# Kernel tuning notes

Measured on AMD Instinct MI355X. Metric: run time of the kernel, lower is better.

The kernel has to match this reference:

```python
import jax, jax.numpy as jnp
import numpy as np

N, E, F_IN, H, C = 50000, 800000, 128, 4, 73
HC = H * C  # 292
NEG_SLOPE_ATT = 0.2   # GATv2 attention leaky relu
NEG_SLOPE_ACT = 0.01  # F.leaky_relu default
BN_EPS = 1e-5


def setup_inputs() -> dict:
    key = jax.random.key(0)
    ks = jax.random.split(key, 20)
    rn = lambda k, shp, s=0.05: (jax.random.normal(k, shp, jnp.float32) * s)
    inp = {
        'x': jax.random.normal(ks[0], (N, F_IN), jnp.float32),
        'edge_index': jax.random.randint(ks[1], (2, E), 0, N, jnp.int64),
        # conv1 (in=F_IN)
        'Wl1': rn(ks[2], (HC, F_IN)), 'bl1': rn(ks[3], (HC,)),
        'Wr1': rn(ks[4], (HC, F_IN)), 'br1': rn(ks[5], (HC,)),
        'att1': rn(ks[6], (H, C)), 'b1': rn(ks[7], (HC,)),
        # conv2 (in=HC)
        'Wl2': rn(ks[8], (HC, HC)), 'bl2': rn(ks[9], (HC,)),
        'Wr2': rn(ks[10], (HC, HC)), 'br2': rn(ks[11], (HC,)),
        'att2': rn(ks[12], (H, C)), 'b2': rn(ks[13], (HC,)),
        # shared BatchNorm1d(HC)
        'gamma': jnp.ones((HC,), jnp.float32), 'beta': jnp.zeros((HC,), jnp.float32),
        # classifier Linear(HC, 2)
        'Wc': rn(ks[14], (2, HC)), 'bc': rn(ks[15], (2,)),
    }
    return inp


def _gatv2(x, src, dst, Wl, bl, Wr, br, att, b):
    # lin_l on source, lin_r on target (PyG GATv2Conv, share_weights=False)
    xl = (x @ Wl.T + bl).reshape(-1, H, C)  # [N,H,C]
    xr = (x @ Wr.T + br).reshape(-1, H, C)
    f = xl[src] + xr[dst]                    # [E,H,C] edge-wise gather
    s = jnp.einsum('ehc,hc->eh', jax.nn.leaky_relu(f, NEG_SLOPE_ATT), att)
    # segment softmax over incoming edges of each destination node
    m = jax.ops.segment_max(s, dst, num_segments=N)
    ex = jnp.exp(s - m[dst])
    den = jax.ops.segment_sum(ex, dst, num_segments=N)
    alpha = ex / (den[dst] + 1e-16)          # [E,H]
    out = jax.ops.segment_sum(alpha[:, :, None] * xl[src], dst, num_segments=N)
    return out.reshape(-1, HC) + b           # concat heads + bias


def _bn(x, gamma, beta):
    mu = jnp.mean(x, axis=0)
    var = jnp.mean((x - mu) ** 2, axis=0)
    return (x - mu) * jax.lax.rsqrt(var + BN_EPS) * gamma + beta


def reference(x, edge_index, Wl1, bl1, Wr1, br1, att1, b1,
              Wl2, bl2, Wr2, br2, att2, b2, gamma, beta, Wc, bc):
    src, dst = edge_index[0], edge_index[1]
    h = _gatv2(x, src, dst, Wl1, bl1, Wr1, br1, att1, b1)
    h = jax.nn.leaky_relu(_bn(h, gamma, beta), NEG_SLOPE_ACT)
    h = _gatv2(h, src, dst, Wl2, bl2, Wr2, br2, att2, b2)
    h = jax.nn.leaky_relu(_bn(h, gamma, beta), NEG_SLOPE_ACT)
    return h @ Wc.T + bc
```

## Files before the change

kernel.cpp:

```cpp
#include <hip/hip_runtime.h>

#define HCDIM 292
#define NHEAD 4
#define CDIM 73
#define SLOTS 5
#define NPERM 320
#define BN_EPS 1e-5f

using u16x8 = __attribute__((ext_vector_type(8))) unsigned short;
using s16x8 = __attribute__((ext_vector_type(8))) short;
using f32x4 = __attribute__((ext_vector_type(4))) float;
using u16x4 = __attribute__((ext_vector_type(4))) unsigned short;

__device__ inline ushort f2bf(float f) {
  unsigned int u = __float_as_uint(f);
  u += 0x7FFFu + ((u >> 16) & 1u);
  return (ushort)(u >> 16);
}
__device__ inline float bf2f(ushort v) {
  return __uint_as_float(((unsigned int)v) << 16);
}

__device__ inline int perm2feat(int p, bool& valid) {
  int h, c;
  if (p < 256) {
    h = p >> 6;
    c = ((p & 3) << 4) | ((p >> 2) & 15);
    valid = true;
  } else {
    int q = p - 256;
    h = q >> 4;
    c = 64 + (q & 15);
    valid = (q & 15) < (CDIM - 64);
  }
  return h * CDIM + c;
}

__global__ void k_wperm(const float* __restrict__ W, const float* __restrict__ b,
                        ushort* __restrict__ Wp, float* __restrict__ pb,
                        int Kin, int Kpad, int kperm) {
  int p = blockIdx.x, t = threadIdx.x;
  bool pv;
  int gn = perm2feat(p, pv);
  int gk = t;
  bool kv = t < Kin;
  if (kperm) { bool v2; gk = perm2feat(t, v2); kv = v2; }
  ushort v = 0;
  if (pv && kv) v = f2bf(W[(size_t)gn * Kin + gk]);
  Wp[(size_t)p * Kpad + t] = v;
  if (t == 0) pb[p] = pv ? b[gn] : 0.f;
}

__global__ void k_vecperm(const float* __restrict__ att1, const float* __restrict__ b1,
                          const float* __restrict__ att2, const float* __restrict__ b2,
                          const float* __restrict__ gamma, const float* __restrict__ beta,
                          const float* __restrict__ Wc, float* __restrict__ o) {
  int p = threadIdx.x, w = blockIdx.x;
  bool pv;
  int gn = perm2feat(p, pv);
  const float* src;
  switch (w) {
    case 0: src = att1; break;
    case 1: src = b1; break;
    case 2: src = att2; break;
    case 3: src = b2; break;
    case 4: src = gamma; break;
    case 5: src = beta; break;
    case 6: src = Wc; break;
    default: src = Wc + HCDIM; break;
  }
  o[w * NPERM + p] = pv ? src[gn] : 0.f;
}

__global__ void k_hist(const int* __restrict__ dst, int* __restrict__ deg, int E) {
  int i = blockIdx.x * blockDim.x + threadIdx.x;
  if (i < E) atomicAdd(&deg[dst[i]], 1);
}

__global__ __launch_bounds__(256) void k_block_sum(const int* __restrict__ deg,
                                                   int* __restrict__ bsum, int n) {
  __shared__ int s[256];
  int i = blockIdx.x * 256 + threadIdx.x;
  s[threadIdx.x] = (i < n) ? deg[i] : 0;
  __syncthreads();
  for (int off = 128; off > 0; off >>= 1) {
    if (threadIdx.x < off) s[threadIdx.x] += s[threadIdx.x + off];
    __syncthreads();
  }
  if (threadIdx.x == 0) bsum[blockIdx.x] = s[0];
}

__global__ __launch_bounds__(256) void k_scan_small(const int* __restrict__ bsum,
                                                    int* __restrict__ boff, int G) {
  __shared__ int s[256];
  int t = threadIdx.x;
  int v = (t < G) ? bsum[t] : 0;
  s[t] = v;
  __syncthreads();
  for (int off = 1; off < 256; off <<= 1) {
    int tv = (t >= off) ? s[t - off] : 0;
    __syncthreads();
    s[t] += tv;
    __syncthreads();
  }
  if (t < G) boff[t] = s[t] - v;
}

__global__ __launch_bounds__(256) void k_scan_final(const int* __restrict__ deg,
                                                    const int* __restrict__ boff,
                                                    int* __restrict__ row_ptr,
                                                    int* __restrict__ cursor,
                                                    int n, int E) {
  __shared__ int s[256];
  int t = threadIdx.x;
  int i = blockIdx.x * 256 + t;
  int v = (i < n) ? deg[i] : 0;
  s[t] = v;
  __syncthreads();
  for (int off = 1; off < 256; off <<= 1) {
    int tv = (t >= off) ? s[t - off] : 0;
    __syncthreads();
    s[t] += tv;
    __syncthreads();
  }
  if (i < n) {
    int rp = boff[blockIdx.x] + s[t] - v;
    row_ptr[i] = rp;
    cursor[i] = rp;
  }
  if (i == 0) row_ptr[n] = E;
}

__global__ void k_csr_fill(const int* __restrict__ srcs, const int* __restrict__ dsts,
                           int* __restrict__ cursor, int* __restrict__ csr_src, int E) {
  int i = blockIdx.x * blockDim.x + threadIdx.x;
  if (i < E) {
    int pos = atomicAdd(&cursor[dsts[i]], 1);
    csr_src[pos] = srcs[i];
  }
}

template <bool CVT>
__device__ inline void load_af(const char* const (&Ar)[4], int koff, int quad,
                               s16x8 (&af)[4]) {
#pragma unroll
  for (int i = 0; i < 4; ++i) {
    if (CVT) {
      const float* p = (const float*)Ar[i] + koff + quad * 8;
      float4 f0 = *(const float4*)p;
      float4 f1 = *(const float4*)(p + 4);
      s16x8 v;
      v[0] = (short)f2bf(f0.x); v[1] = (short)f2bf(f0.y);
      v[2] = (short)f2bf(f0.z); v[3] = (short)f2bf(f0.w);
      v[4] = (short)f2bf(f1.x); v[5] = (short)f2bf(f1.y);
      v[6] = (short)f2bf(f1.z); v[7] = (short)f2bf(f1.w);
      af[i] = v;
    } else {
      af[i] = *(const s16x8*)((const ushort*)Ar[i] + koff + quad * 8);
    }
  }
}

template <int KS, bool CVT>
__global__ __launch_bounds__(256) void k_gemm_blds(
    const void* __restrict__ Av, const ushort* __restrict__ Wb,
    const float* __restrict__ pb, ushort* __restrict__ o0,
    ushort* __restrict__ o1, int M, int miters) {
  constexpr int KSTEPS = KS / 32;
  constexpr int BSTR = KS + 8;
  __shared__ ushort Bs[80 * BSTR];
  int b = blockIdx.x;
  int mlo = b & 7, ct = (b >> 3) & 7, mhi = b >> 6;
  int mc = mlo + 8 * mhi;
  ushort* out = (ct < 4) ? o0 : o1;
  const int colbase = (ct & 3) * 80;
  const int tid = threadIdx.x;
  const int wave = tid >> 6, lane = tid & 63;
  const int quad = lane >> 4, lr = lane & 15;
  const int esz = CVT ? 4 : 2;

  for (int idx = tid; idx < 80 * (KS / 8); idx += 256) {
    int r = idx / (KS / 8), c8 = idx - r * (KS / 8);
    *(u16x8*)(Bs + r * BSTR + c8 * 8) =
        *(const u16x8*)(Wb + (size_t)(ct * 80 + r) * KS + c8 * 8);
  }
  __syncthreads();

  const ushort* bp[5];
#pragma unroll
  for (int i = 0; i < 5; ++i) bp[i] = Bs + (i * 16 + lr) * BSTR;

  float4 pbv[5];
#pragma unroll
  for (int ni = 0; ni < 5; ++ni)
    pbv[ni] = *(const float4*)(pb + ct * 80 + ni * 16 + quad * 4);

  for (int it = mc; it < miters; it += 64) {
    int mbase = it * 256 + wave * 64;
    const char* Ar[4];
#pragma unroll
    for (int i = 0; i < 4; ++i) {
      int ar = mbase + i * 16 + lr;
      if (ar >= M) ar = M - 1;
      Ar[i] = (const char*)Av + (size_t)ar * KS * esz;
    }
    f32x4 acc[4][5] = {};
    s16x8 afb[2][4];
    load_af<CVT>(Ar, 0, quad, afb[0]);
#pragma unroll
    for (int s = 0; s < KSTEPS; ++s) {
      if (s + 1 < KSTEPS) load_af<CVT>(Ar, (s + 1) * 32, quad, afb[(s + 1) & 1]);
      s16x8 bf[5];
#pragma unroll
      for (int i = 0; i < 5; ++i)
        bf[i] = *(const s16x8*)(bp[i] + s * 32 + quad * 8);
#pragma unroll
      for (int ni = 0; ni < 5; ++ni)
#pragma unroll
        for (int mi = 0; mi < 4; ++mi)
          acc[mi][ni] = __builtin_amdgcn_mfma_f32_16x16x32_bf16(
              bf[ni], afb[s & 1][mi], acc[mi][ni], 0, 0, 0);
    }
#pragma unroll
    for (int mi = 0; mi < 4; ++mi) {
      int gm = mbase + mi * 16 + lr;
      if (gm >= M) continue;
      ushort* orow = out + (size_t)gm * NPERM + colbase + quad * 4;
#pragma unroll
      for (int ni = 0; ni < 5; ++ni) {
        u16x4 o;
        o[0] = f2bf(acc[mi][ni][0] + pbv[ni].x);
        o[1] = f2bf(acc[mi][ni][1] + pbv[ni].y);
        o[2] = f2bf(acc[mi][ni][2] + pbv[ni].z);
        o[3] = f2bf(acc[mi][ni][3] + pbv[ni].w);
        *(u16x4*)(orow + ni * 16) = o;
      }
    }
  }
}

__global__ __launch_bounds__(256) void k_pre(const ushort* __restrict__ xl,
                                             const float* __restrict__ attp,
                                             float* __restrict__ pl, int n) {
  int wave = threadIdx.x >> 6, lane = threadIdx.x & 63;
  int d = blockIdx.x * 4 + wave;
  if (d >= n) return;
  int hgrp = lane >> 4, li = lane & 15;
  u16x4 a4 = *(const u16x4*)(xl + (size_t)d * NPERM + lane * 4);
  ushort a1 = xl[(size_t)d * NPERM + 256 + lane];
  float Ta = 0.f;
#pragma unroll
  for (int k = 0; k < 4; ++k) Ta = fmaf(bf2f(a4[k]), attp[lane * 4 + k], Ta);
  Ta = fmaf(bf2f(a1), attp[256 + lane], Ta);
#pragma unroll
  for (int off = 1; off < 16; off <<= 1) Ta += __shfl_xor(Ta, off, 64);
  if (li == 0) pl[d * 4 + hgrp] = 0.6f * Ta;
}

__global__ __launch_bounds__(256) void k_agg(const ushort* __restrict__ xl,
                                             const ushort* __restrict__ xr,
                                             const float* __restrict__ pl,
                                             const int* __restrict__ csr_src,
                                             const int* __restrict__ row_ptr,
                                             const float* __restrict__ attp,
                                             const float* __restrict__ bp,
                                             ushort* __restrict__ out, int n) {
  int wave = threadIdx.x >> 6, lane = threadIdx.x & 63;
  int d = blockIdx.x * 4 + wave;
  if (d >= n) return;
  int hgrp = lane >> 4;
  int start = __builtin_amdgcn_readfirstlane(row_ptr[d]);
  int end = __builtin_amdgcn_readfirstlane(row_ptr[d + 1]);

  float bpv[SLOTS];
#pragma unroll
  for (int k = 0; k < 4; ++k) bpv[k] = bp[lane * 4 + k];
  bpv[4] = bp[256 + lane];

  if (start >= end) {
    u16x4 o4;
#pragma unroll
    for (int k = 0; k < 4; ++k) o4[k] = f2bf(bpv[k]);
    *(u16x4*)(out + (size_t)d * NPERM + lane * 4) = o4;
    out[(size_t)d * NPERM + 256 + lane] = f2bf(bpv[4]);
    return;
  }

  float xrv[SLOTS], attv[SLOTS], acc[SLOTS] = {};
  {
    u16x4 r4 = *(const u16x4*)(xr + (size_t)d * NPERM + lane * 4);
#pragma unroll
    for (int k = 0; k < 4; ++k) {
      xrv[k] = bf2f(r4[k]);
      attv[k] = 0.4f * attp[lane * 4 + k];
    }
    xrv[4] = bf2f(xr[(size_t)d * NPERM + 256 + lane]);
    attv[4] = 0.4f * attp[256 + lane];
  }
  float Tb = 0.f;
#pragma unroll
  for (int k = 0; k < SLOTS; ++k) Tb = fmaf(xrv[k], attv[k], Tb);
  Tb += __shfl_xor(Tb, 1, 64);
  Tb += __shfl_xor(Tb, 2, 64);
  Tb += __shfl_xor(Tb, 4, 64);
  Tb += __shfl_xor(Tb, 8, 64);
  float prv = 1.5f * Tb;
  float den = 0.f;
  int dg = end - start;

  int sA = __builtin_amdgcn_readfirstlane(csr_src[start]);
  int eB0 = (dg > 1) ? start + 1 : start;
  int sB = __builtin_amdgcn_readfirstlane(csr_src[eB0]);
  u16x4 a4 = *(const u16x4*)(xl + (size_t)sA * NPERM + lane * 4);
  ushort a1 = xl[(size_t)sA * NPERM + 256 + lane];
  float plA = pl[sA * 4 + hgrp];
  u16x4 b4 = *(const u16x4*)(xl + (size_t)sB * NPERM + lane * 4);
  ushort b1 = xl[(size_t)sB * NPERM + 256 + lane];
  float plB = pl[sB * 4 + hgrp];

  for (int e = start; e + 1 < end; e += 2) {
    int p0 = (e + 2 < end) ? e + 2 : end - 1;
    int p1 = (e + 3 < end) ? e + 3 : end - 1;
    int t0 = __builtin_amdgcn_readfirstlane(csr_src[p0]);
    int t1 = __builtin_amdgcn_readfirstlane(csr_src[p1]);
    u16x4 n4a = *(const u16x4*)(xl + (size_t)t0 * NPERM + lane * 4);
    ushort n1a = xl[(size_t)t0 * NPERM + 256 + lane];
    float plN0 = pl[t0 * 4 + hgrp];
    u16x4 n4b = *(const u16x4*)(xl + (size_t)t1 * NPERM + lane * 4);
    ushort n1b = xl[(size_t)t1 * NPERM + 256 + lane];
    float plN1 = pl[t1 * 4 + hgrp];

    float xa[SLOTS] = {bf2f(a4[0]), bf2f(a4[1]), bf2f(a4[2]), bf2f(a4[3]), bf2f(a1)};
    float xb[SLOTS] = {bf2f(b4[0]), bf2f(b4[1]), bf2f(b4[2]), bf2f(b4[3]), bf2f(b1)};
    float Ta = 0.f, Tc = 0.f;
#pragma unroll
    for (int k = 0; k < SLOTS; ++k) {
      Ta = fmaf(fabsf(xa[k] + xrv[k]), attv[k], Ta);
      Tc = fmaf(fabsf(xb[k] + xrv[k]), attv[k], Tc);
    }
    Ta += __shfl_xor(Ta, 1, 64);  Tc += __shfl_xor(Tc, 1, 64);
    Ta += __shfl_xor(Ta, 2, 64);  Tc += __shfl_xor(Tc, 2, 64);
    Ta += __shfl_xor(Ta, 4, 64);  Tc += __shfl_xor(Tc, 4, 64);
    Ta += __shfl_xor(Ta, 8, 64);  Tc += __shfl_xor(Tc, 8, 64);
    float sa_ = fminf(Ta + plA + prv, 60.f);
    float sb_ = fminf(Tc + plB + prv, 60.f);
    float wa = __expf(sa_);
    float wb = __expf(sb_);
    den += wa + wb;
#pragma unroll
    for (int k = 0; k < SLOTS; ++k) {
      acc[k] = fmaf(wa, xa[k], acc[k]);
      acc[k] = fmaf(wb, xb[k], acc[k]);
    }
    a4 = n4a; a1 = n1a; plA = plN0;
    b4 = n4b; b1 = n1b; plB = plN1;
  }

  if (dg & 1) {
    float xa[SLOTS] = {bf2f(a4[0]), bf2f(a4[1]), bf2f(a4[2]), bf2f(a4[3]), bf2f(a1)};
    float Ta = 0.f;
#pragma unroll
    for (int k = 0; k < SLOTS; ++k)
      Ta = fmaf(fabsf(xa[k] + xrv[k]), attv[k], Ta);
    Ta += __shfl_xor(Ta, 1, 64);
    Ta += __shfl_xor(Ta, 2, 64);
    Ta += __shfl_xor(Ta, 4, 64);
    Ta += __shfl_xor(Ta, 8, 64);
    float wa = __expf(fminf(Ta + plA + prv, 60.f));
    den += wa;
#pragma unroll
    for (int k = 0; k < SLOTS; ++k) acc[k] = fmaf(wa, xa[k], acc[k]);
  }

  float inv = 1.f / (den + 1e-16f);
  u16x4 o4;
#pragma unroll
  for (int k = 0; k < 4; ++k) o4[k] = f2bf(fmaf(acc[k], inv, bpv[k]));
  *(u16x4*)(out + (size_t)d * NPERM + lane * 4) = o4;
  out[(size_t)d * NPERM + 256 + lane] = f2bf(fmaf(acc[4], inv, bpv[4]));
}

__global__ __launch_bounds__(320) void k_bn_reduce(const ushort* __restrict__ h,
                                                   float* __restrict__ colsum,
                                                   float* __restrict__ colsq,
                                                   int n, int rows_per_block) {
  int c = threadIdx.x;
  int r0 = blockIdx.x * rows_per_block;
  int r1 = min(r0 + rows_per_block, n);
  float s = 0.f, s2 = 0.f;
  for (int r = r0; r < r1; ++r) {
    float v = bf2f(h[(size_t)r * NPERM + c]);
    s += v;
    s2 += v * v;
  }
  atomicAdd(&colsum[c], s);
  atomicAdd(&colsq[c], s2);
}

__global__ void k_bn_coef(float* __restrict__ colsum, float* __restrict__ colsq,
                          const float* __restrict__ gp, const float* __restrict__ bp,
                          float invN) {
  int c = threadIdx.x + blockIdx.x * blockDim.x;
  if (c >= NPERM) return;
  float mu = colsum[c] * invN;
  float var = colsq[c] * invN - mu * mu;
  float scale = rsqrtf(var + BN_EPS) * gp[c];
  colsum[c] = scale;
  colsq[c] = bp[c] - mu * scale;
}

__global__ void k_bn_apply_bf(const ushort* __restrict__ h,
                              const float* __restrict__ scale,
                              const float* __restrict__ shift,
                              ushort* __restrict__ outb, int total8) {
  int i = blockIdx.x * blockDim.x + threadIdx.x;
  if (i >= total8) return;
  int cg = i - (i / 40) * 40;
  u16x8 v = *(const u16x8*)(h + (size_t)i * 8);
  u16x8 o;
#pragma unroll
  for (int k = 0; k < 8; ++k) {
    int c = cg * 8 + k;
    float f = fmaf(bf2f(v[k]), scale[c], shift[c]);
    f = (f > 0.f) ? f : 0.01f * f;
    o[k] = f2bf(f);
  }
  *(u16x8*)(outb + (size_t)i * 8) = o;
}

__global__ __launch_bounds__(256) void k_bn_classifier(
    const ushort* __restrict__ h, const float* __restrict__ scale,
    const float* __restrict__ shift, const float* __restrict__ wc0,
    const float* __restrict__ wc1, const float* __restrict__ bc,
    float* __restrict__ out, int n) {
  int wave = threadIdx.x >> 6, lane = threadIdx.x & 63;
  int r = blockIdx.x * 4 + wave;
  if (r >= n) return;
  float a0 = 0.f, a1 = 0.f;
#pragma unroll
  for (int k = 0; k < SLOTS; ++k) {
    int slot = lane + 64 * k;
    float v = fmaf(bf2f(h[(size_t)r * NPERM + slot]), scale[slot], shift[slot]);
    v = (v > 0.f) ? v : 0.01f * v;
    a0 = fmaf(v, wc0[slot], a0);
    a1 = fmaf(v, wc1[slot], a1);
  }
#pragma unroll
  for (int off = 32; off > 0; off >>= 1) {
    a0 += __shfl_xor(a0, off, 64);
    a1 += __shfl_xor(a1, off, 64);
  }
  if (lane == 0) {
    out[(size_t)2 * r] = a0 + bc[0];
    out[(size_t)2 * r + 1] = a1 + bc[1];
  }
}

extern "C" void kernel_launch(void* const* d_in, const int* in_sizes, int n_in,
                              void* d_out, int out_size, void* d_ws, size_t ws_size,
                              hipStream_t stream) {
  const float* x      = (const float*)d_in[0];
  const int*   eidx   = (const int*)d_in[1];
  const float* Wl1    = (const float*)d_in[2];
  const float* bl1    = (const float*)d_in[3];
  const float* Wr1    = (const float*)d_in[4];
  const float* br1    = (const float*)d_in[5];
  const float* att1   = (const float*)d_in[6];
  const float* b1     = (const float*)d_in[7];
  const float* Wl2    = (const float*)d_in[8];
  const float* bl2    = (const float*)d_in[9];
  const float* Wr2    = (const float*)d_in[10];
  const float* br2    = (const float*)d_in[11];
  const float* att2   = (const float*)d_in[12];
  const float* b2     = (const float*)d_in[13];
  const float* gamma  = (const float*)d_in[14];
  const float* beta   = (const float*)d_in[15];
  const float* Wc     = (const float*)d_in[16];
  const float* bc     = (const float*)d_in[17];
  float* out = (float*)d_out;

  const int FIN = 128;
  const int N = in_sizes[0] / FIN;
  const int E = in_sizes[1] / 2;

  const int* src = eidx;
  const int* dst = eidx + E;

  ushort* h      = (ushort*)d_ws;
  ushort* xl     = h + (size_t)N * NPERM;
  ushort* xr     = xl + (size_t)N * NPERM;
  ushort* abuf   = xr + (size_t)N * NPERM;
  ushort* wb     = abuf + (size_t)N * NPERM;
  float* pb      = (float*)(wb + (size_t)2 * NPERM * NPERM);
  float* vecp    = pb + 2 * NPERM;
  float* pl      = vecp + 8 * NPERM;
  float* colsum  = pl + (size_t)N * NHEAD;
  float* colsq   = colsum + NPERM;
  int* deg       = (int*)(colsq + NPERM);
  int* row_ptr   = deg + N;
  int* cursor    = row_ptr + N + 1;
  int* bsum      = cursor + N;
  int* boff      = bsum + 256;
  int* csr_src   = boff + 256;

  const int G = (N + 255) / 256;
  const int EB = (E + 255) / 256;
  const int AGGB = (N + 3) / 4;
  const int MITERS = (N + 255) / 256;
  const int GEMMB = 512;

  const float* att1p = vecp;
  const float* b1p   = vecp + NPERM;
  const float* att2p = vecp + 2 * NPERM;
  const float* b2p   = vecp + 3 * NPERM;
  const float* gp    = vecp + 4 * NPERM;
  const float* btp   = vecp + 5 * NPERM;
  const float* wc0   = vecp + 6 * NPERM;
  const float* wc1   = vecp + 7 * NPERM;

  hipMemsetAsync(deg, 0, (size_t)N * sizeof(int), stream);
  k_hist<<<EB, 256, 0, stream>>>(dst, deg, E);
  k_block_sum<<<G, 256, 0, stream>>>(deg, bsum, N);
  k_scan_small<<<1, 256, 0, stream>>>(bsum, boff, G);
  k_scan_final<<<G, 256, 0, stream>>>(deg, boff, row_ptr, cursor, N, E);
  k_csr_fill<<<EB, 256, 0, stream>>>(src, dst, cursor, csr_src, E);

  k_vecperm<<<8, NPERM, 0, stream>>>(att1, b1, att2, b2, gamma, beta, Wc, vecp);

  k_wperm<<<NPERM, FIN, 0, stream>>>(Wl1, bl1, wb, pb, FIN, FIN, 0);
  k_wperm<<<NPERM, FIN, 0, stream>>>(Wr1, br1, wb + (size_t)NPERM * FIN, pb + NPERM,
                                     FIN, FIN, 0);
  k_gemm_blds<FIN, true><<<GEMMB, 256, 0, stream>>>((const void*)x, wb, pb,
                                                    xl, xr, N, MITERS);
  k_pre<<<AGGB, 256, 0, stream>>>(xl, att1p, pl, N);
  k_agg<<<AGGB, 256, 0, stream>>>(xl, xr, pl, csr_src, row_ptr, att1p, b1p, h, N);

  const int RPB = (N + 255) / 256;
  hipMemsetAsync(colsum, 0, 2 * NPERM * sizeof(float), stream);
  k_bn_reduce<<<256, NPERM, 0, stream>>>(h, colsum, colsq, N, RPB);
  k_bn_coef<<<2, 160, 0, stream>>>(colsum, colsq, gp, btp, 1.f / (float)N);
  k_bn_apply_bf<<<(N * 40 + 255) / 256, 256, 0, stream>>>(h, colsum, colsq, abuf,
                                                          N * 40);

  k_wperm<<<NPERM, NPERM, 0, stream>>>(Wl2, bl2, wb, pb, HCDIM, NPERM, 1);
  k_wperm<<<NPERM, NPERM, 0, stream>>>(Wr2, br2, wb + (size_t)NPERM * NPERM,
                                       pb + NPERM, HCDIM, NPERM, 1);
  k_gemm_blds<NPERM, false><<<GEMMB, 256, 0, stream>>>((const void*)abuf, wb, pb,
                                                       xl, xr, N, MITERS);
  k_pre<<<AGGB, 256, 0, stream>>>(xl, att2p, pl, N);
  k_agg<<<AGGB, 256, 0, stream>>>(xl, xr, pl, csr_src, row_ptr, att2p, b2p, h, N);

  hipMemsetAsync(colsum, 0, 2 * NPERM * sizeof(float), stream);
  k_bn_reduce<<<256, NPERM, 0, stream>>>(h, colsum, colsq, N, RPB);
  k_bn_coef<<<2, 160, 0, stream>>>(colsum, colsq, gp, btp, 1.f / (float)N);

  k_bn_classifier<<<AGGB, 256, 0, stream>>>(h, colsum, colsq, wc0, wc1, bc, out, N);
}
```

Measured before the change: 635.2 us.

## Switch intermediate storage and MFMA from bf16 to fp16 with packed dot math

Changes every stored intermediate (weights, projected features, aggregated outputs) from bf16 to fp16. The GEMMs now use fp16 MFMA and packed round-toward-zero conversion instead of manual bf16 rounding. The attention logits in the aggregation kernel use packed half adds, abs via bitmask and fdot2, and the softmax uses exp2 with log2e folded into the attention vector. This cuts conversion and ALU instructions in the edge loop. The trade-off is fp16 range and precision risk on activations, and the exp clamp threshold changes.

```diff
diff --git a/kernel.cpp b/kernel.cpp
--- a/kernel.cpp
+++ b/kernel.cpp
@@ -6,19 +6,32 @@
 #define SLOTS 5
 #define NPERM 320
 #define BN_EPS 1e-5f
+#define LOG2E 1.44269504f
 
 using u16x8 = __attribute__((ext_vector_type(8))) unsigned short;
-using s16x8 = __attribute__((ext_vector_type(8))) short;
 using f32x4 = __attribute__((ext_vector_type(4))) float;
 using u16x4 = __attribute__((ext_vector_type(4))) unsigned short;
-
-__device__ inline ushort f2bf(float f) {
-  unsigned int u = __float_as_uint(f);
-  u += 0x7FFFu + ((u >> 16) & 1u);
-  return (ushort)(u >> 16);
-}
-__device__ inline float bf2f(ushort v) {
-  return __uint_as_float(((unsigned int)v) << 16);
+using hf2   = __attribute__((ext_vector_type(2))) _Float16;
+using v2h   = __attribute__((ext_vector_type(2))) __fp16;
+using v8h   = __attribute__((ext_vector_type(8))) __fp16;
+
+__device__ inline v2h pkrtz(float a, float b) {
+  return __builtin_amdgcn_cvt_pkrtz(a, b);
+}
+__device__ inline float fdot2(hf2 a, hf2 b, float c) {
+  return __builtin_amdgcn_fdot2(__builtin_bit_cast(v2h, a),
+                                __builtin_bit_cast(v2h, b), c, false);
+}
+__device__ inline ushort f2h(float f) {
+  _Float16 h = (_Float16)f;
+  return __builtin_bit_cast(ushort, h);
+}
+__device__ inline float h2f(ushort v) {
+  return (float)__builtin_bit_cast(_Float16, v);
+}
+__device__ inline hf2 habs2(hf2 a) {
+  unsigned u = __builtin_bit_cast(unsigned, a) & 0x7fff7fffu;
+  return __builtin_bit_cast(hf2, u);
 }
 
 __device__ inline int perm2feat(int p, bool& valid) {
@@ -46,7 +59,7 @@
   bool kv = t < Kin;
   if (kperm) { bool v2; gk = perm2feat(t, v2); kv = v2; }
   ushort v = 0;
-  if (pv && kv) v = f2bf(W[(size_t)gn * Kin + gk]);
+  if (pv && kv) v = f2h(W[(size_t)gn * Kin + gk]);
   Wp[(size_t)p * Kpad + t] = v;
   if (t == 0) pb[p] = pv ? b[gn] : 0.f;
 }
@@ -142,21 +155,21 @@
 
 template <bool CVT>
 __device__ inline void load_af(const char* const (&Ar)[4], int koff, int quad,
-                               s16x8 (&af)[4]) {
+                               v8h (&af)[4]) {
 #pragma unroll
   for (int i = 0; i < 4; ++i) {
     if (CVT) {
       const float* p = (const float*)Ar[i] + koff + quad * 8;
       float4 f0 = *(const float4*)p;
       float4 f1 = *(const float4*)(p + 4);
-      s16x8 v;
-      v[0] = (short)f2bf(f0.x); v[1] = (short)f2bf(f0.y);
-      v[2] = (short)f2bf(f0.z); v[3] = (short)f2bf(f0.w);
-      v[4] = (short)f2bf(f1.x); v[5] = (short)f2bf(f1.y);
-      v[6] = (short)f2bf(f1.z); v[7] = (short)f2bf(f1.w);
-      af[i] = v;
+      union { v2h h[4]; v8h v; } u;
+      u.h[0] = pkrtz(f0.x, f0.y);
+      u.h[1] = pkrtz(f0.z, f0.w);
+      u.h[2] = pkrtz(f1.x, f1.y);
+      u.h[3] = pkrtz(f1.z, f1.w);
+      af[i] = u.v;
     } else {
-      af[i] = *(const s16x8*)((const ushort*)Ar[i] + koff + quad * 8);
+      af[i] = *(const v8h*)((const ushort*)Ar[i] + koff + quad * 8);
     }
   }
 }
@@ -205,20 +218,20 @@
       Ar[i] = (const char*)Av + (size_t)ar * KS * esz;
     }
     f32x4 acc[4][5] = {};
-    s16x8 afb[2][4];
+    v8h afb[2][4];
     load_af<CVT>(Ar, 0, quad, afb[0]);
 #pragma unroll
     for (int s = 0; s < KSTEPS; ++s) {
       if (s + 1 < KSTEPS) load_af<CVT>(Ar, (s + 1) * 32, quad, afb[(s + 1) & 1]);
-      s16x8 bf[5];
+      v8h bf[5];
 #pragma unroll
       for (int i = 0; i < 5; ++i)
-        bf[i] = *(const s16x8*)(bp[i] + s * 32 + quad * 8);
+        bf[i] = *(const v8h*)(bp[i] + s * 32 + quad * 8);
 #pragma unroll
       for (int ni = 0; ni < 5; ++ni)
 #pragma unroll
         for (int mi = 0; mi < 4; ++mi)
-          acc[mi][ni] = __builtin_amdgcn_mfma_f32_16x16x32_bf16(
+          acc[mi][ni] = __builtin_amdgcn_mfma_f32_16x16x32_f16(
               bf[ni], afb[s & 1][mi], acc[mi][ni], 0, 0, 0);
     }
 #pragma unroll
@@ -228,12 +241,10 @@
       ushort* orow = out + (size_t)gm * NPERM + colbase + quad * 4;
 #pragma unroll
       for (int ni = 0; ni < 5; ++ni) {
-        u16x4 o;
-        o[0] = f2bf(acc[mi][ni][0] + pbv[ni].x);
-        o[1] = f2bf(acc[mi][ni][1] + pbv[ni].y);
-        o[2] = f2bf(acc[mi][ni][2] + pbv[ni].z);
-        o[3] = f2bf(acc[mi][ni][3] + pbv[ni].w);
-        *(u16x4*)(orow + ni * 16) = o;
+        union { v2h h[2]; u16x4 o; } u;
+        u.h[0] = pkrtz(acc[mi][ni][0] + pbv[ni].x, acc[mi][ni][1] + pbv[ni].y);
+        u.h[1] = pkrtz(acc[mi][ni][2] + pbv[ni].z, acc[mi][ni][3] + pbv[ni].w);
+        *(u16x4*)(orow + ni * 16) = u.o;
       }
     }
   }
@@ -246,15 +257,22 @@
   int d = blockIdx.x * 4 + wave;
   if (d >= n) return;
   int hgrp = lane >> 4, li = lane & 15;
-  u16x4 a4 = *(const u16x4*)(xl + (size_t)d * NPERM + lane * 4);
-  ushort a1 = xl[(size_t)d * NPERM + 256 + lane];
-  float Ta = 0.f;
-#pragma unroll
-  for (int k = 0; k < 4; ++k) Ta = fmaf(bf2f(a4[k]), attp[lane * 4 + k], Ta);
-  Ta = fmaf(bf2f(a1), attp[256 + lane], Ta);
+  const float C = 0.4f * LOG2E;
+  float4 a4 = *(const float4*)(attp + lane * 4);
+  hf2 av01{(_Float16)(C * a4.x), (_Float16)(C * a4.y)};
+  hf2 av23{(_Float16)(C * a4.z), (_Float16)(C * a4.w)};
+  hf2 av5{(_Float16)(C * attp[256 + lane]), (_Float16)0.f};
+
+  uint2 cc = *(const uint2*)(xl + (size_t)d * NPERM + lane * 4);
+  ushort c5 = xl[(size_t)d * NPERM + 256 + lane];
+  hf2 c01 = __builtin_bit_cast(hf2, cc.x);
+  hf2 c23 = __builtin_bit_cast(hf2, cc.y);
+  hf2 c5h{__builtin_bit_cast(_Float16, c5), (_Float16)0.f};
+
+  float Ta = fdot2(c01, av01, fdot2(c23, av23, fdot2(c5h, av5, 0.f)));
 #pragma unroll
   for (int off = 1; off < 16; off <<= 1) Ta += __shfl_xor(Ta, off, 64);
-  if (li == 0) pl[d * 4 + hgrp] = 0.6f * Ta;
+  if (li == 0) pl[d * 4 + hgrp] = 1.5f * Ta;
 }
 
 __global__ __launch_bounds__(256) void k_agg(const ushort* __restrict__ xl,
@@ -272,49 +290,49 @@
   int start = __builtin_amdgcn_readfirstlane(row_ptr[d]);
   int end = __builtin_amdgcn_readfirstlane(row_ptr[d + 1]);
 
-  float bpv[SLOTS];
-#pragma unroll
-  for (int k = 0; k < 4; ++k) bpv[k] = bp[lane * 4 + k];
-  bpv[4] = bp[256 + lane];
+  float4 bp4 = *(const float4*)(bp + lane * 4);
+  float bp5 = bp[256 + lane];
 
   if (start >= end) {
-    u16x4 o4;
-#pragma unroll
-    for (int k = 0; k < 4; ++k) o4[k] = f2bf(bpv[k]);
-    *(u16x4*)(out + (size_t)d * NPERM + lane * 4) = o4;
-    out[(size_t)d * NPERM + 256 + lane] = f2bf(bpv[4]);
+    union { v2h h[2]; u16x4 o; } u;
+    u.h[0] = pkrtz(bp4.x, bp4.y);
+    u.h[1] = pkrtz(bp4.z, bp4.w);
+    *(u16x4*)(out + (size_t)d * NPERM + lane * 4) = u.o;
+    out[(size_t)d * NPERM + 256 + lane] = f2h(bp5);
     return;
   }
 
-  float xrv[SLOTS], attv[SLOTS], acc[SLOTS] = {};
+  const float C = 0.4f * LOG2E;
+  float4 at4 = *(const float4*)(attp + lane * 4);
+  hf2 av01{(_Float16)(C * at4.x), (_Float16)(C * at4.y)};
+  hf2 av23{(_Float16)(C * at4.z), (_Float16)(C * at4.w)};
+  hf2 av5{(_Float16)(C * attp[256 + lane]), (_Float16)0.f};
+
+  hf2 xr01, xr23, xr5;
   {
-    u16x4 r4 = *(const u16x4*)(xr + (size_t)d * NPERM + lane * 4);
-#pragma unroll
-    for (int k = 0; k < 4; ++k) {
-      xrv[k] = bf2f(r4[k]);
-      attv[k] = 0.4f * attp[lane * 4 + k];
-    }
-    xrv[4] = bf2f(xr[(size_t)d * NPERM + 256 + lane]);
-    attv[4] = 0.4f * attp[256 + lane];
-  }
-  float Tb = 0.f;
-#pragma unroll
-  for (int k = 0; k < SLOTS; ++k) Tb = fmaf(xrv[k], attv[k], Tb);
+    uint2 rr = *(const uint2*)(xr + (size_t)d * NPERM + lane * 4);
+    xr01 = __builtin_bit_cast(hf2, rr.x);
+    xr23 = __builtin_bit_cast(hf2, rr.y);
+    xr5 = hf2{__builtin_bit_cast(_Float16, xr[(size_t)d * NPERM + 256 + lane]),
+              (_Float16)0.f};
+  }
+  float Tb = fdot2(xr01, av01, fdot2(xr23, av23, fdot2(xr5, av5, 0.f)));
   Tb += __shfl_xor(Tb, 1, 64);
   Tb += __shfl_xor(Tb, 2, 64);
   Tb += __shfl_xor(Tb, 4, 64);
   Tb += __shfl_xor(Tb, 8, 64);
   float prv = 1.5f * Tb;
+  float acc[SLOTS] = {};
   float den = 0.f;
   int dg = end - start;
 
   int sA = __builtin_amdgcn_readfirstlane(csr_src[start]);
   int eB0 = (dg > 1) ? start + 1 : start;
   int sB = __builtin_amdgcn_readfirstlane(csr_src[eB0]);
-  u16x4 a4 = *(const u16x4*)(xl + (size_t)sA * NPERM + lane * 4);
+  uint2 a8 = *(const uint2*)(xl + (size_t)sA * NPERM + lane * 4);
   ushort a1 = xl[(size_t)sA * NPERM + 256 + lane];
   float plA = pl[sA * 4 + hgrp];
-  u16x4 b4 = *(const u16x4*)(xl + (size_t)sB * NPERM + lane * 4);
+  uint2 b8 = *(const uint2*)(xl + (size_t)sB * NPERM + lane * 4);
   ushort b1 = xl[(size_t)sB * NPERM + 256 + lane];
   float plB = pl[sB * 4 + hgrp];
 
@@ -323,61 +341,70 @@
     int p1 = (e + 3 < end) ? e + 3 : end - 1;
     int t0 = __builtin_amdgcn_readfirstlane(csr_src[p0]);
     int t1 = __builtin_amdgcn_readfirstlane(csr_src[p1]);
-    u16x4 n4a = *(const u16x4*)(xl + (size_t)t0 * NPERM + lane * 4);
+    uint2 n8a = *(const uint2*)(xl + (size_t)t0 * NPERM + lane * 4);
     ushort n1a = xl[(size_t)t0 * NPERM + 256 + lane];
     float plN0 = pl[t0 * 4 + hgrp];
-    u16x4 n4b = *(const u16x4*)(xl + (size_t)t1 * NPERM + lane * 4);
+    uint2 n8b = *(const uint2*)(xl + (size_t)t1 * NPERM + lane * 4);
     ushort n1b = xl[(size_t)t1 * NPERM + 256 + lane];
     float plN1 = pl[t1 * 4 + hgrp];
 
-    float xa[SLOTS] = {bf2f(a4[0]), bf2f(a4[1]), bf2f(a4[2]), bf2f(a4[3]), bf2f(a1)};
-    float xb[SLOTS] = {bf2f(b4[0]), bf2f(b4[1]), bf2f(b4[2]), bf2f(b4[3]), bf2f(b1)};
-    float Ta = 0.f, Tc = 0.f;
-#pragma unroll
-    for (int k = 0; k < SLOTS; ++k) {
-      Ta = fmaf(fabsf(xa[k] + xrv[k]), attv[k], Ta);
-      Tc = fmaf(fabsf(xb[k] + xrv[k]), attv[k], Tc);
-    }
+    hf2 a01 = __builtin_bit_cast(hf2, a8.x), a23 = __builtin_bit_cast(hf2, a8.y);
+    hf2 a5{__builtin_bit_cast(_Float16, a1), (_Float16)0.f};
+    hf2 c01 = __builtin_bit_cast(hf2, b8.x), c23 = __builtin_bit_cast(hf2, b8.y);
+    hf2 c5{__builtin_bit_cast(_Float16, b1), (_Float16)0.f};
+
+    float Ta = fdot2(habs2(a01 + xr01), av01,
+               fdot2(habs2(a23 + xr23), av23,
+               fdot2(habs2(a5 + xr5), av5, 0.f)));
+    float Tc = fdot2(habs2(c01 + xr01), av01,
+               fdot2(habs2(c23 + xr23), av23,
+               fdot2(habs2(c5 + xr5), av5, 0.f)));
     Ta += __shfl_xor(Ta, 1, 64);  Tc += __shfl_xor(Tc, 1, 64);
     Ta += __shfl_xor(Ta, 2, 64);  Tc += __shfl_xor(Tc, 2, 64);
     Ta += __shfl_xor(Ta, 4, 64);  Tc += __shfl_xor(Tc, 4, 64);
     Ta += __shfl_xor(Ta, 8, 64);  Tc += __shfl_xor(Tc, 8, 64);
-    float sa_ = fminf(Ta + plA + prv, 60.f);
-    float sb_ = fminf(Tc + plB + prv, 60.f);
-    float wa = __expf(sa_);
-    float wb = __expf(sb_);
+    float wa = exp2f(fminf(Ta + plA + prv, 80.f));
+    float wb = exp2f(fminf(Tc + plB + prv, 80.f));
     den += wa + wb;
-#pragma unroll
-    for (int k = 0; k < SLOTS; ++k) {
-      acc[k] = fmaf(wa, xa[k], acc[k]);
-      acc[k] = fmaf(wb, xb[k], acc[k]);
-    }
-    a4 = n4a; a1 = n1a; plA = plN0;
-    b4 = n4b; b1 = n1b; plB = plN1;
+    acc[0] = fmaf(wa, (float)a01[0], acc[0]);
+    acc[1] = fmaf(wa, (float)a01[1], acc[1]);
+    acc[2] = fmaf(wa, (float)a23[0], acc[2]);
+    acc[3] = fmaf(wa, (float)a23[1], acc[3]);
+    acc[4] = fmaf(wa, (float)a5[0], acc[4]);
+    acc[0] = fmaf(wb, (float)c01[0], acc[0]);
+    acc[1] = fmaf(wb, (float)c01[1], acc[1]);
+    acc[2] = fmaf(wb, (float)c23[0], acc[2]);
+    acc[3] = fmaf(wb, (float)c23[1], acc[3]);
+    acc[4] = fmaf(wb, (float)c5[0], acc[4]);
+    a8 = n8a; a1 = n1a; plA = plN0;
+    b8 = n8b; b1 = n1b; plB = plN1;
   }
 
   if (dg & 1) {
-    float xa[SLOTS] = {bf2f(a4[0]), bf2f(a4[1]), bf2f(a4[2]), bf2f(a4[3]), bf2f(a1)};
-    float Ta = 0.f;
-#pragma unroll
-    for (int k = 0; k < SLOTS; ++k)
-      Ta = fmaf(fabsf(xa[k] + xrv[k]), attv[k], Ta);
+    hf2 a01 = __builtin_bit_cast(hf2, a8.x), a23 = __builtin_bit_cast(hf2, a8.y);
+    hf2 a5{__builtin_bit_cast(_Float16, a1), (_Float16)0.f};
+    float Ta = fdot2(habs2(a01 + xr01), av01,
+               fdot2(habs2(a23 + xr23), av23,
+               fdot2(habs2(a5 + xr5), av5, 0.f)));
     Ta += __shfl_xor(Ta, 1, 64);
     Ta += __shfl_xor(Ta, 2, 64);
     Ta += __shfl_xor(Ta, 4, 64);
     Ta += __shfl_xor(Ta, 8, 64);
-    float wa = __expf(fminf(Ta + plA + prv, 60.f));
+    float wa = exp2f(fminf(Ta + plA + prv, 80.f));
     den += wa;
-#pragma unroll
-    for (int k = 0; k < SLOTS; ++k) acc[k] = fmaf(wa, xa[k], acc[k]);
+    acc[0] = fmaf(wa, (float)a01[0], acc[0]);
+    acc[1] = fmaf(wa, (float)a01[1], acc[1]);
+    acc[2] = fmaf(wa, (float)a23[0], acc[2]);
+    acc[3] = fmaf(wa, (float)a23[1], acc[3]);
+    acc[4] = fmaf(wa, (float)a5[0], acc[4]);
   }
 
   float inv = 1.f / (den + 1e-16f);
-  u16x4 o4;
-#pragma unroll
-  for (int k = 0; k < 4; ++k) o4[k] = f2bf(fmaf(acc[k], inv, bpv[k]));
-  *(u16x4*)(out + (size_t)d * NPERM + lane * 4) = o4;
-  out[(size_t)d * NPERM + 256 + lane] = f2bf(fmaf(acc[4], inv, bpv[4]));
+  union { v2h h[2]; u16x4 o; } u;
+  u.h[0] = pkrtz(fmaf(acc[0], inv, bp4.x), fmaf(acc[1], inv, bp4.y));
+  u.h[1] = pkrtz(fmaf(acc[2], inv, bp4.z), fmaf(acc[3], inv, bp4.w));
+  *(u16x4*)(out + (size_t)d * NPERM + lane * 4) = u.o;
+  out[(size_t)d * NPERM + 256 + lane] = f2h(fmaf(acc[4], inv, bp5));
 }
 
 __global__ __launch_bounds__(320) void k_bn_reduce(const ushort* __restrict__ h,
@@ -389,7 +416,7 @@
   int r1 = min(r0 + rows_per_block, n);
   float s = 0.f, s2 = 0.f;
   for (int r = r0; r < r1; ++r) {
-    float v = bf2f(h[(size_t)r * NPERM + c]);
+    float v = h2f(h[(size_t)r * NPERM + c]);
     s += v;
     s2 += v * v;
   }
@@ -417,15 +444,18 @@
   if (i >= total8) return;
   int cg = i - (i / 40) * 40;
   u16x8 v = *(const u16x8*)(h + (size_t)i * 8);
-  u16x8 o;
+  float f[8];
 #pragma unroll
   for (int k = 0; k < 8; ++k) {
     int c = cg * 8 + k;
-    float f = fmaf(bf2f(v[k]), scale[c], shift[c]);
-    f = (f > 0.f) ? f : 0.01f * f;
-    o[k] = f2bf(f);
-  }
-  *(u16x8*)(outb + (size_t)i * 8) = o;
+    float t = fmaf(h2f(v[k]), scale[c], shift[c]);
+    f[k] = (t > 0.f) ? t : 0.01f * t;
+  }
+  union { v2h h4[4]; u16x8 o; } u;
+#pragma unroll
+  for (int k = 0; k < 4; ++k)
+    u.h4[k] = pkrtz(f[2 * k], f[2 * k + 1]);
+  *(u16x8*)(outb + (size_t)i * 8) = u.o;
 }
 
 __global__ __launch_bounds__(256) void k_bn_classifier(
@@ -440,7 +470,7 @@
 #pragma unroll
   for (int k = 0; k < SLOTS; ++k) {
     int slot = lane + 64 * k;
-    float v = fmaf(bf2f(h[(size_t)r * NPERM + slot]), scale[slot], shift[slot]);
+    float v = fmaf(h2f(h[(size_t)r * NPERM + slot]), scale[slot], shift[slot]);
     v = (v > 0.f) ? v : 0.01f * v;
     a0 = fmaf(v, wc0[slot], a0);
     a1 = fmaf(v, wc1[slot], a1);
```

Result: no change. 627.0 us (-1.3%).
